# Performance work log

Hardware: AMD Instinct MI355X
Metric: run time of the kernel (lower is better)

The kernel has to match this reference:

```python
import jax, jax.numpy as jnp
import numpy as np

ETYPES = [0, 2, 1]          # indexes into doubled RotatE0 r_vec (2*R rows)
OUT_DIM = 64
NUM_HEADS = 8
ALPHA = 0.01                # LeakyReLU slope
R = 2                       # raw relation count (r_vec rows before doubling)
N = 100000                  # num nodes
E = 250000                  # num edges (metapath instances)
L = len(ETYPES) + 1         # metapath length


def setup_inputs() -> dict:
    key = jax.random.key(0)
    k = jax.random.split(key, 6)
    features = jax.random.normal(k[0], (N, OUT_DIM), jnp.float32)
    r_vec = jax.random.normal(k[1], (R, OUT_DIM // 2, 2), jnp.float32)
    attn1_w = jax.random.normal(k[2], (NUM_HEADS, OUT_DIM), jnp.float32) * 0.1
    attn2 = jax.random.normal(k[3], (1, NUM_HEADS, OUT_DIM), jnp.float32) * 0.1
    edge_metapath_indices = jax.random.randint(k[4], (E, L), 0, N)
    edge_dst = jax.random.randint(k[5], (E,), 0, N)
    return {"features": features, "r_vec": r_vec, "attn1_w": attn1_w,
            "attn2": attn2, "edge_metapath_indices": edge_metapath_indices,
            "edge_dst": edge_dst}


def _forward(features, r_vec, attn1_w, attn2, edge_metapath_indices, edge_dst):
    D2 = OUT_DIM // 2
    # --- RotatE0 relation vectors: normalize each complex pair to unit length ---
    rv = r_vec / jnp.linalg.norm(r_vec, axis=2, keepdims=True)      # [R, D2, 2]
    rv_conj = rv * jnp.array([1.0, -1.0], rv.dtype)                 # conjugate
    rv2 = jnp.stack((rv, rv_conj), axis=1).reshape(2 * R, D2, 2)    # [2R, D2, 2]
    # --- cumulative rotation per metapath position (reverse product) ---
    fr = [None] * L
    fr[L - 1] = jnp.stack([jnp.ones(D2, rv.dtype), jnp.zeros(D2, rv.dtype)], -1)
    for i in range(L - 2, -1, -1):
        if ETYPES[i] is not None:
            r = rv2[ETYPES[i]]                                       # [D2, 2]
            re = fr[i + 1][:, 0] * r[:, 0] - fr[i + 1][:, 1] * r[:, 1]
            im = fr[i + 1][:, 0] * r[:, 1] + fr[i + 1][:, 1] * r[:, 0]
            fr[i] = jnp.stack([re, im], axis=-1)
        else:
            fr[i] = fr[i + 1]
    frv = jnp.stack(fr, axis=0)                                      # [L, D2, 2]
    # --- gather node features along each metapath instance ---
    edata = features[edge_metapath_indices]                          # [E, L, D]
    ed = edata.reshape(edata.shape[0], L, D2, 2)
    # position L-1 has identity rotation (1,0), so rotate all positions at once
    re = ed[..., 0] * frv[None, :, :, 0] - ed[..., 1] * frv[None, :, :, 1]
    im = ed[..., 0] * frv[None, :, :, 1] + ed[..., 1] * frv[None, :, :, 0]
    ed = jnp.stack([re, im], axis=-1).reshape(edata.shape[0], L, OUT_DIM)
    hidden = ed.mean(axis=1)                                         # [E, D]
    eft = jnp.tile(hidden, (1, NUM_HEADS)).reshape(-1, NUM_HEADS, OUT_DIM)
    # --- attention scores (attn_switch=True) ---
    center = features[edge_metapath_indices[:, -1]]                  # [E, D]
    a1 = center @ attn1_w.T                                          # [E, H]
    a2 = (eft * attn2).sum(axis=-1)                                  # [E, H]
    a = a1 + a2
    a = jnp.where(a > 0, a, ALPHA * a)[:, :, None]                   # leaky relu, [E,H,1]
    # --- edge softmax over destination-node segments ---
    amax = jax.lax.stop_gradient(jax.ops.segment_max(a, edge_dst, num_segments=N))
    aexp = jnp.exp(a - amax[edge_dst])
    asum = jax.ops.segment_sum(aexp, edge_dst, num_segments=N)
    attn = aexp / asum[edge_dst]                                     # [E, H, 1]
    # --- message passing: weighted scatter-sum to destination nodes ---
    h = jax.ops.segment_sum(eft * attn, edge_dst, num_segments=N)    # [N, H, D]
    return h


def reference(features, r_vec, attn1_w, attn2, edge_metapath_indices, edge_dst):
    return _forward(features, r_vec, attn1_w, attn2, edge_metapath_indices, edge_dst)
```

## Files before the change

### kernel.cpp

```cpp
#include <hip/hip_runtime.h>

#define NUM_HEADS 8

__global__ void k_frv(const float2* __restrict__ rvec, float2* __restrict__ frv) {
    int d = threadIdx.x;
    if (d >= 32) return;
    float2 a = rvec[d];
    float2 b = rvec[32 + d];
    float na = rsqrtf(a.x*a.x + a.y*a.y); a.x *= na; a.y *= na;
    float nb = rsqrtf(b.x*b.x + b.y*b.y); b.x *= nb; b.y *= nb;
    float2 fr3 = make_float2(1.f, 0.f);
    float2 fr2 = make_float2(a.x, -a.y);
    float2 fr1 = make_float2(fr2.x*b.x - fr2.y*b.y, fr2.x*b.y + fr2.y*b.x);
    float2 fr0 = make_float2(fr1.x*a.x - fr1.y*a.y, fr1.x*a.y + fr1.y*a.x);
    frv[d] = fr0; frv[32+d] = fr1; frv[64+d] = fr2; frv[96+d] = fr3;
}

__global__ __launch_bounds__(256) void k_edge(
    const float2* __restrict__ feat,
    const float2* __restrict__ frv_g,
    const float2* __restrict__ w1_g,
    const float2* __restrict__ w2_g,
    const int4*   __restrict__ emi,
    const int*    __restrict__ edge_dst,
    float2*       __restrict__ hidden,
    float*        __restrict__ a_buf,
    unsigned*     __restrict__ amax,
    int*          __restrict__ counts,
    int E)
{
    __shared__ float2 s_frv[96];
    __shared__ float2 s_w1[256];
    __shared__ float2 s_w2[256];
    int tid = threadIdx.x;
    if (tid < 96) s_frv[tid] = frv_g[tid];
    s_w1[tid] = w1_g[tid];
    s_w2[tid] = w2_g[tid];
    __syncthreads();

    int e = blockIdx.x * 8 + (tid >> 5);
    if (e >= E) return;
    int lane = tid & 31;

    int4 idx = emi[e];
    float2 f0 = feat[(size_t)idx.x * 32 + lane];
    float2 f1 = feat[(size_t)idx.y * 32 + lane];
    float2 f2 = feat[(size_t)idx.z * 32 + lane];
    float2 c3 = feat[(size_t)idx.w * 32 + lane];

    float2 acc = c3;
    float2 q;
    q = s_frv[lane];      acc.x += f0.x*q.x - f0.y*q.y; acc.y += f0.x*q.y + f0.y*q.x;
    q = s_frv[32+lane];   acc.x += f1.x*q.x - f1.y*q.y; acc.y += f1.x*q.y + f1.y*q.x;
    q = s_frv[64+lane];   acc.x += f2.x*q.x - f2.y*q.y; acc.y += f2.x*q.y + f2.y*q.x;
    float2 h = make_float2(acc.x * 0.25f, acc.y * 0.25f);
    hidden[(size_t)e * 32 + lane] = h;

    float p[NUM_HEADS];
    #pragma unroll
    for (int hh = 0; hh < NUM_HEADS; ++hh) {
        float2 w1 = s_w1[hh*32 + lane], w2 = s_w2[hh*32 + lane];
        p[hh] = c3.x*w1.x + c3.y*w1.y + h.x*w2.x + h.y*w2.y;
    }
    #pragma unroll
    for (int hh = 0; hh < NUM_HEADS; ++hh) {
        #pragma unroll
        for (int off = 16; off > 0; off >>= 1)
            p[hh] += __shfl_xor(p[hh], off, 32);
    }
    if (lane == 0) {
        int dst = edge_dst[e];
        atomicAdd(&counts[dst], 1);
        #pragma unroll
        for (int hh = 0; hh < NUM_HEADS; ++hh) {
            float a = p[hh];
            a = a > 0.f ? a : 0.01f * a;
            a_buf[(size_t)e * 8 + hh] = a;
            unsigned enc = __float_as_uint(a);
            enc = (enc & 0x80000000u) ? ~enc : (enc | 0x80000000u);
            atomicMax(&amax[(size_t)dst * 8 + hh], enc);
        }
    }
}

__global__ __launch_bounds__(256) void k_scan_a(
    const int* __restrict__ counts, int* __restrict__ offsets,
    int* __restrict__ blocksums, int N)
{
    __shared__ int s[256];
    int t = threadIdx.x;
    int base = blockIdx.x * 1024 + t * 4;
    int v0 = (base     < N) ? counts[base]     : 0;
    int v1 = (base + 1 < N) ? counts[base + 1] : 0;
    int v2 = (base + 2 < N) ? counts[base + 2] : 0;
    int v3 = (base + 3 < N) ? counts[base + 3] : 0;
    s[t] = v0 + v1 + v2 + v3;
    __syncthreads();
    #pragma unroll
    for (int off = 1; off < 256; off <<= 1) {
        int x = (t >= off) ? s[t - off] : 0;
        __syncthreads();
        s[t] += x;
        __syncthreads();
    }
    if (t == 255) blocksums[blockIdx.x] = s[255];
    int run = (t == 0) ? 0 : s[t - 1];
    if (base     < N) offsets[base]     = run; run += v0;
    if (base + 1 < N) offsets[base + 1] = run; run += v1;
    if (base + 2 < N) offsets[base + 2] = run; run += v2;
    if (base + 3 < N) offsets[base + 3] = run;
}

__global__ __launch_bounds__(1024) void k_scan_b(
    int* __restrict__ blocksums, int* __restrict__ total, int B)
{
    __shared__ int s[1024];
    int t = threadIdx.x;
    s[t] = (t < B) ? blocksums[t] : 0;
    __syncthreads();
    #pragma unroll
    for (int off = 1; off < 1024; off <<= 1) {
        int x = (t >= off) ? s[t - off] : 0;
        __syncthreads();
        s[t] += x;
        __syncthreads();
    }
    if (t < B) blocksums[t] = (t == 0) ? 0 : s[t - 1];
    if (t == 1023) *total = s[1023];
}

__global__ __launch_bounds__(256) void k_scan_c(
    int* __restrict__ offsets, int* __restrict__ cursor,
    const int* __restrict__ blocksums, const int* __restrict__ total, int N)
{
    int i = blockIdx.x * 256 + threadIdx.x;
    if (i < N) {
        int v = offsets[i] + blocksums[i >> 10];
        offsets[i] = v;
        cursor[i] = v;
    }
    if (i == 0) offsets[N] = *total;
}

__global__ void k_fill(const int* __restrict__ edge_dst, int* __restrict__ cursor,
                       int* __restrict__ edge_ids, int E) {
    int e = blockIdx.x * 256 + threadIdx.x;
    if (e >= E) return;
    int pos = atomicAdd(&cursor[edge_dst[e]], 1);
    edge_ids[pos] = e;
}

__global__ void k_soft(const int* __restrict__ edge_dst,
                       const unsigned* __restrict__ amax,
                       float* __restrict__ a_buf,
                       float* __restrict__ asum,
                       int total) {
    int i = blockIdx.x * 256 + threadIdx.x;
    if (i >= total) return;
    int e = i >> 3, hh = i & 7;
    int dst = edge_dst[e];
    unsigned enc = amax[dst * 8 + hh];
    float m = (enc & 0x80000000u) ? __uint_as_float(enc & 0x7fffffffu)
                                  : __uint_as_float(~enc);
    float v = expf(a_buf[i] - m);
    a_buf[i] = v;
    unsafeAtomicAdd(&asum[dst * 8 + hh], v);
}

__global__ __launch_bounds__(256) void k_out(
    const float2* __restrict__ hidden,
    const float*  __restrict__ aexp,
    const float*  __restrict__ asum,
    const int*    __restrict__ offsets,
    const int*    __restrict__ edge_ids,
    float2*       __restrict__ out,
    int N)
{
    int tid = threadIdx.x;
    int n = blockIdx.x * 8 + (tid >> 5);
    if (n >= N) return;
    int lane = tid & 31;
    int beg = offsets[n], end = offsets[n + 1];
    float rinv[NUM_HEADS];
    #pragma unroll
    for (int hh = 0; hh < NUM_HEADS; ++hh)
        rinv[hh] = 1.0f / asum[(size_t)n * 8 + hh];
    float2 acc[NUM_HEADS];
    #pragma unroll
    for (int hh = 0; hh < NUM_HEADS; ++hh) acc[hh] = make_float2(0.f, 0.f);
    for (int j = beg; j < end; ++j) {
        int e = edge_ids[j];
        float2 hv = hidden[(size_t)e * 32 + lane];
        #pragma unroll
        for (int hh = 0; hh < NUM_HEADS; ++hh) {
            float w = aexp[(size_t)e * 8 + hh] * rinv[hh];
            acc[hh].x += hv.x * w;
            acc[hh].y += hv.y * w;
        }
    }
    #pragma unroll
    for (int hh = 0; hh < NUM_HEADS; ++hh)
        out[((size_t)n * 8 + hh) * 32 + lane] = acc[hh];
}

extern "C" void kernel_launch(void* const* d_in, const int* in_sizes, int n_in,
                              void* d_out, int out_size, void* d_ws, size_t ws_size,
                              hipStream_t stream) {
    const float2* feat = (const float2*)d_in[0];
    const float2* rvec = (const float2*)d_in[1];
    const float2* w1   = (const float2*)d_in[2];
    const float2* w2   = (const float2*)d_in[3];
    const int4*   emi  = (const int4*)d_in[4];
    const int* edge_dst = (const int*)d_in[5];

    int N = in_sizes[0] / 64;
    int E = in_sizes[4] / 4;
    int nTiles = (N + 1023) / 1024;

    char* w = (char*)d_ws;
    float2*   frv      = (float2*)w;
    float*    hidden   = (float*)(w + 1024);
    float*    a_buf    = hidden + (size_t)E * 64;
    unsigned* amax     = (unsigned*)(a_buf + (size_t)E * 8);
    float*    asum     = (float*)(amax + (size_t)N * 8);
    int*      counts   = (int*)(asum + (size_t)N * 8);
    int*      offsets  = counts + N;
    int*      cursor   = offsets + N + 1;
    int*      edge_ids = cursor + N;
    int*      blocksums= edge_ids + E;
    int*      total    = blocksums + 1024;

    hipMemsetAsync(amax,   0, (size_t)N * 8 * 4, stream);
    hipMemsetAsync(asum,   0, (size_t)N * 8 * 4, stream);
    hipMemsetAsync(counts, 0, (size_t)N * 4, stream);

    k_frv<<<1, 64, 0, stream>>>(rvec, frv);
    k_edge<<<(E + 7) / 8, 256, 0, stream>>>(feat, frv, w1, w2, emi, edge_dst,
                                            (float2*)hidden, a_buf, amax, counts, E);
    k_scan_a<<<nTiles, 256, 0, stream>>>(counts, offsets, blocksums, N);
    k_scan_b<<<1, 1024, 0, stream>>>(blocksums, total, nTiles);
    k_scan_c<<<(N + 255) / 256, 256, 0, stream>>>(offsets, cursor, blocksums, total, N);
    k_fill<<<(E + 255) / 256, 256, 0, stream>>>(edge_dst, cursor, edge_ids, E);
    k_soft<<<(E * 8 + 255) / 256, 256, 0, stream>>>(edge_dst, amax, a_buf, asum, E * 8);
    k_out<<<(N + 7) / 8, 256, 0, stream>>>((const float2*)hidden, a_buf, asum,
                                           offsets, edge_ids, (float2*)d_out, N);
}
```

Baseline: 407.9 us.

## Fuse edge softmax into CSR gather kernel and drop atomic max/sum pass

New measurement: 374.3 us. 1.09x faster.

```diff
diff --git a/kernel.cpp b/kernel.cpp
--- a/kernel.cpp
+++ b/kernel.cpp
@@ -2,30 +2,19 @@
 
 #define NUM_HEADS 8
 
-__global__ void k_frv(const float2* __restrict__ rvec, float2* __restrict__ frv) {
-    int d = threadIdx.x;
-    if (d >= 32) return;
-    float2 a = rvec[d];
-    float2 b = rvec[32 + d];
-    float na = rsqrtf(a.x*a.x + a.y*a.y); a.x *= na; a.y *= na;
-    float nb = rsqrtf(b.x*b.x + b.y*b.y); b.x *= nb; b.y *= nb;
-    float2 fr3 = make_float2(1.f, 0.f);
-    float2 fr2 = make_float2(a.x, -a.y);
-    float2 fr1 = make_float2(fr2.x*b.x - fr2.y*b.y, fr2.x*b.y + fr2.y*b.x);
-    float2 fr0 = make_float2(fr1.x*a.x - fr1.y*a.y, fr1.x*a.y + fr1.y*a.x);
-    frv[d] = fr0; frv[32+d] = fr1; frv[64+d] = fr2; frv[96+d] = fr3;
+__device__ __forceinline__ float2 cmul(float2 a, float2 b) {
+    return make_float2(a.x*b.x - a.y*b.y, a.x*b.y + a.y*b.x);
 }
 
 __global__ __launch_bounds__(256) void k_edge(
     const float2* __restrict__ feat,
-    const float2* __restrict__ frv_g,
+    const float2* __restrict__ rvec,
     const float2* __restrict__ w1_g,
     const float2* __restrict__ w2_g,
     const int4*   __restrict__ emi,
     const int*    __restrict__ edge_dst,
     float2*       __restrict__ hidden,
     float*        __restrict__ a_buf,
-    unsigned*     __restrict__ amax,
     int*          __restrict__ counts,
     int E)
 {
@@ -33,7 +22,16 @@
     __shared__ float2 s_w1[256];
     __shared__ float2 s_w2[256];
     int tid = threadIdx.x;
-    if (tid < 96) s_frv[tid] = frv_g[tid];
+    if (tid < 32) {
+        float2 a = rvec[tid];
+        float2 b = rvec[32 + tid];
+        float na = rsqrtf(a.x*a.x + a.y*a.y); a.x *= na; a.y *= na;
+        float nb = rsqrtf(b.x*b.x + b.y*b.y); b.x *= nb; b.y *= nb;
+        float2 fr2 = make_float2(a.x, -a.y);
+        float2 fr1 = cmul(fr2, b);
+        float2 fr0 = cmul(fr1, a);
+        s_frv[tid] = fr0; s_frv[32+tid] = fr1; s_frv[64+tid] = fr2;
+    }
     s_w1[tid] = w1_g[tid];
     s_w2[tid] = w2_g[tid];
     __syncthreads();
@@ -62,25 +60,19 @@
         float2 w1 = s_w1[hh*32 + lane], w2 = s_w2[hh*32 + lane];
         p[hh] = c3.x*w1.x + c3.y*w1.y + h.x*w2.x + h.y*w2.y;
     }
+    float myv = 0.f;
     #pragma unroll
     for (int hh = 0; hh < NUM_HEADS; ++hh) {
         #pragma unroll
         for (int off = 16; off > 0; off >>= 1)
             p[hh] += __shfl_xor(p[hh], off, 32);
-    }
-    if (lane == 0) {
-        int dst = edge_dst[e];
-        atomicAdd(&counts[dst], 1);
-        #pragma unroll
-        for (int hh = 0; hh < NUM_HEADS; ++hh) {
-            float a = p[hh];
-            a = a > 0.f ? a : 0.01f * a;
-            a_buf[(size_t)e * 8 + hh] = a;
-            unsigned enc = __float_as_uint(a);
-            enc = (enc & 0x80000000u) ? ~enc : (enc | 0x80000000u);
-            atomicMax(&amax[(size_t)dst * 8 + hh], enc);
-        }
-    }
+        if (lane == hh) myv = p[hh];
+    }
+    if (lane < NUM_HEADS) {
+        float a = myv > 0.f ? myv : 0.01f * myv;
+        a_buf[(size_t)e * 8 + lane] = a;
+    }
+    if (lane == 0) atomicAdd(&counts[edge_dst[e]], 1);
 }
 
 __global__ __launch_bounds__(256) void k_scan_a(
@@ -150,27 +142,9 @@
     edge_ids[pos] = e;
 }
 
-__global__ void k_soft(const int* __restrict__ edge_dst,
-                       const unsigned* __restrict__ amax,
-                       float* __restrict__ a_buf,
-                       float* __restrict__ asum,
-                       int total) {
-    int i = blockIdx.x * 256 + threadIdx.x;
-    if (i >= total) return;
-    int e = i >> 3, hh = i & 7;
-    int dst = edge_dst[e];
-    unsigned enc = amax[dst * 8 + hh];
-    float m = (enc & 0x80000000u) ? __uint_as_float(enc & 0x7fffffffu)
-                                  : __uint_as_float(~enc);
-    float v = expf(a_buf[i] - m);
-    a_buf[i] = v;
-    unsafeAtomicAdd(&asum[dst * 8 + hh], v);
-}
-
 __global__ __launch_bounds__(256) void k_out(
     const float2* __restrict__ hidden,
-    const float*  __restrict__ aexp,
-    const float*  __restrict__ asum,
+    const float*  __restrict__ a_buf,
     const int*    __restrict__ offsets,
     const int*    __restrict__ edge_ids,
     float2*       __restrict__ out,
@@ -181,26 +155,56 @@
     if (n >= N) return;
     int lane = tid & 31;
     int beg = offsets[n], end = offsets[n + 1];
-    float rinv[NUM_HEADS];
-    #pragma unroll
-    for (int hh = 0; hh < NUM_HEADS; ++hh)
-        rinv[hh] = 1.0f / asum[(size_t)n * 8 + hh];
+
+    if (beg == end) {
+        float2 z = make_float2(0.f, 0.f);
+        #pragma unroll
+        for (int hh = 0; hh < NUM_HEADS; ++hh)
+            out[((size_t)n * 8 + hh) * 32 + lane] = z;
+        return;
+    }
+
+    const float4* a4 = (const float4*)a_buf;
+    float4 m0 = make_float4(-1e30f, -1e30f, -1e30f, -1e30f);
+    float4 m1 = m0;
+    for (int j = beg; j < end; ++j) {
+        int e = edge_ids[j];
+        float4 x0 = a4[(size_t)e * 2], x1 = a4[(size_t)e * 2 + 1];
+        m0.x = fmaxf(m0.x, x0.x); m0.y = fmaxf(m0.y, x0.y);
+        m0.z = fmaxf(m0.z, x0.z); m0.w = fmaxf(m0.w, x0.w);
+        m1.x = fmaxf(m1.x, x1.x); m1.y = fmaxf(m1.y, x1.y);
+        m1.z = fmaxf(m1.z, x1.z); m1.w = fmaxf(m1.w, x1.w);
+    }
+    float4 d0 = make_float4(0.f, 0.f, 0.f, 0.f), d1 = d0;
     float2 acc[NUM_HEADS];
     #pragma unroll
     for (int hh = 0; hh < NUM_HEADS; ++hh) acc[hh] = make_float2(0.f, 0.f);
     for (int j = beg; j < end; ++j) {
         int e = edge_ids[j];
+        float4 x0 = a4[(size_t)e * 2], x1 = a4[(size_t)e * 2 + 1];
+        float w0x = __expf(x0.x - m0.x), w0y = __expf(x0.y - m0.y);
+        float w0z = __expf(x0.z - m0.z), w0w = __expf(x0.w - m0.w);
+        float w1x = __expf(x1.x - m1.x), w1y = __expf(x1.y - m1.y);
+        float w1z = __expf(x1.z - m1.z), w1w = __expf(x1.w - m1.w);
+        d0.x += w0x; d0.y += w0y; d0.z += w0z; d0.w += w0w;
+        d1.x += w1x; d1.y += w1y; d1.z += w1z; d1.w += w1w;
         float2 hv = hidden[(size_t)e * 32 + lane];
-        #pragma unroll
-        for (int hh = 0; hh < NUM_HEADS; ++hh) {
-            float w = aexp[(size_t)e * 8 + hh] * rinv[hh];
-            acc[hh].x += hv.x * w;
-            acc[hh].y += hv.y * w;
-        }
-    }
-    #pragma unroll
-    for (int hh = 0; hh < NUM_HEADS; ++hh)
-        out[((size_t)n * 8 + hh) * 32 + lane] = acc[hh];
+        acc[0].x += hv.x * w0x; acc[0].y += hv.y * w0x;
+        acc[1].x += hv.x * w0y; acc[1].y += hv.y * w0y;
+        acc[2].x += hv.x * w0z; acc[2].y += hv.y * w0z;
+        acc[3].x += hv.x * w0w; acc[3].y += hv.y * w0w;
+        acc[4].x += hv.x * w1x; acc[4].y += hv.y * w1x;
+        acc[5].x += hv.x * w1y; acc[5].y += hv.y * w1y;
+        acc[6].x += hv.x * w1z; acc[6].y += hv.y * w1z;
+        acc[7].x += hv.x * w1w; acc[7].y += hv.y * w1w;
+    }
+    float r[NUM_HEADS] = {1.f/d0.x, 1.f/d0.y, 1.f/d0.z, 1.f/d0.w,
+                          1.f/d1.x, 1.f/d1.y, 1.f/d1.z, 1.f/d1.w};
+    #pragma unroll
+    for (int hh = 0; hh < NUM_HEADS; ++hh) {
+        float2 v = make_float2(acc[hh].x * r[hh], acc[hh].y * r[hh]);
+        out[((size_t)n * 8 + hh) * 32 + lane] = v;
+    }
 }
 
 extern "C" void kernel_launch(void* const* d_in, const int* in_sizes, int n_in,
@@ -218,30 +222,23 @@
     int nTiles = (N + 1023) / 1024;
 
     char* w = (char*)d_ws;
-    float2*   frv      = (float2*)w;
-    float*    hidden   = (float*)(w + 1024);
+    float*    hidden   = (float*)w;
     float*    a_buf    = hidden + (size_t)E * 64;
-    unsigned* amax     = (unsigned*)(a_buf + (size_t)E * 8);
-    float*    asum     = (float*)(amax + (size_t)N * 8);
-    int*      counts   = (int*)(asum + (size_t)N * 8);
+    int*      counts   = (int*)(a_buf + (size_t)E * 8);
     int*      offsets  = counts + N;
     int*      cursor   = offsets + N + 1;
     int*      edge_ids = cursor + N;
     int*      blocksums= edge_ids + E;
     int*      total    = blocksums + 1024;
 
-    hipMemsetAsync(amax,   0, (size_t)N * 8 * 4, stream);
-    hipMemsetAsync(asum,   0, (size_t)N * 8 * 4, stream);
     hipMemsetAsync(counts, 0, (size_t)N * 4, stream);
 
-    k_frv<<<1, 64, 0, stream>>>(rvec, frv);
-    k_edge<<<(E + 7) / 8, 256, 0, stream>>>(feat, frv, w1, w2, emi, edge_dst,
-                                            (float2*)hidden, a_buf, amax, counts, E);
+    k_edge<<<(E + 7) / 8, 256, 0, stream>>>(feat, rvec, w1, w2, emi, edge_dst,
+                                            (float2*)hidden, a_buf, counts, E);
     k_scan_a<<<nTiles, 256, 0, stream>>>(counts, offsets, blocksums, N);
     k_scan_b<<<1, 1024, 0, stream>>>(blocksums, total, nTiles);
     k_scan_c<<<(N + 255) / 256, 256, 0, stream>>>(offsets, cursor, blocksums, total, N);
     k_fill<<<(E + 255) / 256, 256, 0, stream>>>(edge_dst, cursor, edge_ids, E);
-    k_soft<<<(E * 8 + 255) / 256, 256, 0, stream>>>(edge_dst, amax, a_buf, asum, E * 8);
-    k_out<<<(N + 7) / 8, 256, 0, stream>>>((const float2*)hidden, a_buf, asum,
+    k_out<<<(N + 7) / 8, 256, 0, stream>>>((const float2*)hidden, a_buf,
                                            offsets, edge_ids, (float2*)d_out, N);
 }
```
